# Kernel tuning notes

Measured on AMD Instinct MI355X. Metric: run time of the kernel, lower is better.

## Reference

```python
import jax, jax.numpy as jnp
import numpy as np

E = 1024      # embedding_size
H = 16        # num_heads
D = E // H    # head dim


def setup_inputs() -> dict:
    key = jax.random.key(0)
    k1, k2, k3, k4, k5 = jax.random.split(key, 5)
    x = jax.random.normal(k1, (4, 2048, E), dtype=jnp.float32)
    # nn.Linear(E, 3E): weight [3E, E], bias [3E]
    w_qkv = jax.random.normal(k2, (3 * E, E), dtype=jnp.float32) * (1.0 / np.sqrt(E))
    b_qkv = jax.random.normal(k3, (3 * E,), dtype=jnp.float32) * 0.02
    # nn.Linear(E, E)
    w_proj = jax.random.normal(k4, (E, E), dtype=jnp.float32) * (1.0 / np.sqrt(E))
    b_proj = jax.random.normal(k5, (E,), dtype=jnp.float32) * 0.02
    return {"x": x, "w_qkv": w_qkv, "b_qkv": b_qkv, "w_proj": w_proj, "b_proj": b_proj}


def reference(x, w_qkv, b_qkv, w_proj, b_proj):
    b, n, _ = x.shape
    qkv = x @ w_qkv.T + b_qkv                       # [b, n, 3E]
    # rearrange 'b n (h d qkv) -> qkv b h n d' : last dim grouped as (h, d, 3)
    qkv = qkv.reshape(b, n, H, D, 3)
    qkv = jnp.transpose(qkv, (4, 0, 2, 1, 3))        # [3, b, h, n, d]
    q, k, v = qkv[0], qkv[1], qkv[2]
    scale = 1.0 / np.sqrt(E / H)
    energy = jnp.einsum('bhqd,bhkd->bhqk', q, k) * scale
    attn = jax.nn.softmax(energy, axis=-1)
    out = jnp.einsum('bhqk,bhkd->bhqd', attn, v)     # [b, h, n, d]
    out = jnp.transpose(out, (0, 2, 1, 3)).reshape(b, n, E)
    return out @ w_proj.T + b_proj
```

## Files before the change

### kernel.cpp

```cpp
#include <hip/hip_runtime.h>
#include <hip/hip_fp16.h>

namespace {

constexpr int B = 4;
constexpr int N = 2048;
constexpr int E = 1024;
constexpr int H = 16;
constexpr int D = 64;
constexpr int M = B * N;

typedef __attribute__((ext_vector_type(8))) short bf16x8;
typedef __attribute__((ext_vector_type(8))) _Float16 f16x8;
typedef __attribute__((ext_vector_type(4))) _Float16 f16x4;
typedef __attribute__((ext_vector_type(4))) float f32x4;

__device__ inline ushort bf16_rne(float f) {
  unsigned u = __float_as_uint(f);
  return (ushort)((u + 0x7FFFu + ((u >> 16) & 1u)) >> 16);
}
__device__ inline void split2(float f, ushort& hi, ushort& lo) {
  unsigned u = __float_as_uint(f);
  hi = (ushort)(u >> 16);
  lo = bf16_rne(f - __uint_as_float(u & 0xFFFF0000u));
}

__global__ __launch_bounds__(256) void split_kernel(
    const float* __restrict__ in, ushort* __restrict__ hi,
    ushort* __restrict__ lo, int n4) {
  int i = blockIdx.x * blockDim.x + threadIdx.x;
  const int stride = gridDim.x * blockDim.x;
  for (; i < n4; i += stride) {
    const float4 f = ((const float4*)in)[i];
    ushort4 h, l;
    split2(f.x, h.x, l.x);
    split2(f.y, h.y, l.y);
    split2(f.z, h.z, l.z);
    split2(f.w, h.w, l.w);
    ((ushort4*)hi)[i] = h;
    ((ushort4*)lo)[i] = l;
  }
}

template <int MODE>
__global__ __launch_bounds__(256) void gemm_x3(
    const ushort* __restrict__ Ahg, const ushort* __restrict__ Alg,
    const ushort* __restrict__ Bhg, const ushort* __restrict__ Blg,
    const float* __restrict__ bias, ushort* __restrict__ qh,
    ushort* __restrict__ ql, ushort* __restrict__ kh, ushort* __restrict__ kl,
    ushort* __restrict__ vt, float* __restrict__ outp) {
  __shared__ ushort LAh[4096], LAl[4096], LBh[4096], LBl[4096];
  const int tid = threadIdx.x;
  const int l = tid & 63, wid = tid >> 6;
  const int wr = wid >> 1, wc = wid & 1;
  const int lr = l & 15, kg = l >> 4;
  const int m0 = blockIdx.x * 128, n0 = blockIdx.y * 128;

  f32x4 acc[4][4];
#pragma unroll
  for (int i = 0; i < 4; ++i)
#pragma unroll
    for (int j = 0; j < 4; ++j) acc[i][j] = (f32x4){0.f, 0.f, 0.f, 0.f};

  for (int k0 = 0; k0 < E; k0 += 32) {
    const ushort* gAh = Ahg + (size_t)m0 * E + k0;
    const ushort* gAl = Alg + (size_t)m0 * E + k0;
    const ushort* gBh = Bhg + (size_t)n0 * E + k0;
    const ushort* gBl = Blg + (size_t)n0 * E + k0;
    __syncthreads();
    auto stage = [&](const ushort* gp, ushort* lp, int half) {
      const int c = half * 256 + tid;
      __builtin_amdgcn_global_load_lds(
          (__attribute__((address_space(1))) void*)(gp + (size_t)(c >> 2) * E +
                                                    (c & 3) * 8),
          (__attribute__((address_space(3))) void*)(lp +
                                                    (half * 256 + (tid & ~63)) * 8),
          16, 0, 0);
    };
    stage(gAh, LAh, 0); stage(gAh, LAh, 1);
    stage(gAl, LAl, 0); stage(gAl, LAl, 1);
    stage(gBh, LBh, 0); stage(gBh, LBh, 1);
    stage(gBl, LBl, 0); stage(gBl, LBl, 1);
    __syncthreads();

    bf16x8 aH[4], aL[4], bH[4], bL[4];
#pragma unroll
    for (int rb = 0; rb < 4; ++rb) {
      const int off = (wr * 64 + rb * 16 + lr) * 32 + kg * 8;
      aH[rb] = *(const bf16x8*)(LAh + off);
      aL[rb] = *(const bf16x8*)(LAl + off);
    }
#pragma unroll
    for (int cb = 0; cb < 4; ++cb) {
      const int off = (wc * 64 + cb * 16 + lr) * 32 + kg * 8;
      bH[cb] = *(const bf16x8*)(LBh + off);
      bL[cb] = *(const bf16x8*)(LBl + off);
    }
#pragma unroll
    for (int rb = 0; rb < 4; ++rb)
#pragma unroll
      for (int cb = 0; cb < 4; ++cb) {
        acc[rb][cb] = __builtin_amdgcn_mfma_f32_16x16x32_bf16(
            aH[rb], bH[cb], acc[rb][cb], 0, 0, 0);
        acc[rb][cb] = __builtin_amdgcn_mfma_f32_16x16x32_bf16(
            aH[rb], bL[cb], acc[rb][cb], 0, 0, 0);
        acc[rb][cb] = __builtin_amdgcn_mfma_f32_16x16x32_bf16(
            aL[rb], bH[cb], acc[rb][cb], 0, 0, 0);
      }
  }

#pragma unroll
  for (int cb = 0; cb < 4; ++cb) {
    const int col = n0 + wc * 64 + cb * 16 + lr;
    const float bv = bias[col];
    if (MODE == 0) {
      const int h = col / 192;
      const int rem = col - h * 192;
      const int dd = rem / 3;
      const int s = rem - dd * 3;
      if (s == 2) {
#pragma unroll
        for (int rb = 0; rb < 4; ++rb) {
          const int m = m0 + wr * 64 + rb * 16 + kg * 4;
          const int bb = m >> 11, nn = m & (N - 1);
          f16x4 pk;
#pragma unroll
          for (int r = 0; r < 4; ++r)
            pk[r] = (_Float16)(acc[rb][cb][r] + bv);
          const size_t vidx =
              ((((size_t)bb * H + h) * (N / 64) + (nn >> 6)) * 64 + dd) * 64 +
              (nn & 63);
          *(f16x4*)((_Float16*)vt + vidx) = pk;
        }
      } else {
#pragma unroll
        for (int rb = 0; rb < 4; ++rb)
#pragma unroll
          for (int r = 0; r < 4; ++r) {
            const int m = m0 + wr * 64 + rb * 16 + kg * 4 + r;
            const int bb = m >> 11, nn = m & (N - 1);
            float v = acc[rb][cb][r] + bv;
            ushort hi, lo;
            const size_t idx = (((size_t)bb * H + h) * N + nn) * D + dd;
            if (s == 0) {
              v *= 0.125f;
              split2(v, hi, lo);
              qh[idx] = hi; ql[idx] = lo;
            } else {
              split2(v, hi, lo);
              kh[idx] = hi; kl[idx] = lo;
            }
          }
      }
    } else {
#pragma unroll
      for (int rb = 0; rb < 4; ++rb)
#pragma unroll
        for (int r = 0; r < 4; ++r) {
          const int m = m0 + wr * 64 + rb * 16 + kg * 4 + r;
          outp[(size_t)m * E + col] = acc[rb][cb][r] + bv;
        }
    }
  }
}

__global__ __launch_bounds__(256, 2) void attn_mfma(
    const ushort* __restrict__ Qh, const ushort* __restrict__ Ql,
    const ushort* __restrict__ Kh, const ushort* __restrict__ Kl,
    const ushort* __restrict__ Vt, ushort* __restrict__ Aoh,
    ushort* __restrict__ Aol) {
  __shared__ ushort KhL[2][4096], KlL[2][4096], VtL[2][4096], PsL[4][4096];
  const int tid = threadIdx.x;
  const int l = tid & 63, w = tid >> 6;
  const int lr = l & 15, g = l >> 4;
  const int bh = blockIdx.x, bb = bh >> 4, hh = bh & 15;
  const int q0 = blockIdx.y * 256 + w * 64;

  const int sr = tid >> 2;
  const int sc = tid & 3;
  const int slotA = sr * 8 + (sc ^ (sr & 7));
  const int slotB = sr * 8 + ((sc + 4) ^ (sr & 7));

  bf16x8 qfh[4][2], qfl[4][2];
#pragma unroll
  for (int rb = 0; rb < 4; ++rb)
#pragma unroll
    for (int ks = 0; ks < 2; ++ks) {
      const size_t off =
          ((size_t)bh * N + q0 + rb * 16 + lr) * D + ks * 32 + g * 8;
      qfh[rb][ks] = *(const bf16x8*)(Qh + off);
      qfl[rb][ks] = *(const bf16x8*)(Ql + off);
    }

  f32x4 o[4][4];
  float m_[4][4], l_[4][4];
#pragma unroll
  for (int rb = 0; rb < 4; ++rb)
#pragma unroll
    for (int r = 0; r < 4; ++r) {
      m_[rb][r] = -1e30f;
      l_[rb][r] = 0.f;
      o[rb][r] = (f32x4){0.f, 0.f, 0.f, 0.f};
    }

  ushort* Pw = &PsL[w][0];
  constexpr int NT = N / 64;

#define LOAD_SET(SET, KT)                                                     \
  do {                                                                        \
    const size_t ko = ((size_t)bh * N + (size_t)(KT) * 64 + sr) * 64;         \
    const size_t vo = (((size_t)bh * (N / 64) + (KT)) * 64 + sr) * 64;        \
    SET[0] = *(const uint4*)(Kh + ko + sc * 8);                               \
    SET[1] = *(const uint4*)(Kh + ko + (sc + 4) * 8);                         \
    SET[2] = *(const uint4*)(Kl + ko + sc * 8);                               \
    SET[3] = *(const uint4*)(Kl + ko + (sc + 4) * 8);                         \
    SET[4] = *(const uint4*)(Vt + vo + sc * 8);                               \
    SET[5] = *(const uint4*)(Vt + vo + (sc + 4) * 8);                         \
  } while (0)

#define WRITE_SET(SET, BUF)                                                   \
  do {                                                                        \
    *(uint4*)(&KhL[BUF][slotA * 8]) = SET[0];                                 \
    *(uint4*)(&KhL[BUF][slotB * 8]) = SET[1];                                 \
    *(uint4*)(&KlL[BUF][slotA * 8]) = SET[2];                                 \
    *(uint4*)(&KlL[BUF][slotB * 8]) = SET[3];                                 \
    *(uint4*)(&VtL[BUF][slotA * 8]) = SET[4];                                 \
    *(uint4*)(&VtL[BUF][slotB * 8]) = SET[5];                                 \
  } while (0)

  auto compute = [&](int buf) {
    const ushort* KhC = &KhL[buf][0];
    const ushort* KlC = &KlL[buf][0];
    const ushort* VtC = &VtL[buf][0];

    f32x4 s4[4][4];
#pragma unroll
    for (int rb = 0; rb < 4; ++rb)
#pragma unroll
      for (int cb = 0; cb < 4; ++cb) s4[rb][cb] = (f32x4){0.f, 0.f, 0.f, 0.f};
    __builtin_amdgcn_s_setprio(1);
#pragma unroll
    for (int ks = 0; ks < 2; ++ks) {
      bf16x8 kfh[4], kfl[4];
#pragma unroll
      for (int cb = 0; cb < 4; ++cb) {
        const int sl = (cb * 16 + lr) * 8 + ((ks * 4 + g) ^ (lr & 7));
        kfh[cb] = *(const bf16x8*)(KhC + sl * 8);
        kfl[cb] = *(const bf16x8*)(KlC + sl * 8);
      }
#pragma unroll
      for (int rb = 0; rb < 4; ++rb)
#pragma unroll
        for (int cb = 0; cb < 4; ++cb) {
          s4[rb][cb] = __builtin_amdgcn_mfma_f32_16x16x32_bf16(
              qfh[rb][ks], kfh[cb], s4[rb][cb], 0, 0, 0);
          s4[rb][cb] = __builtin_amdgcn_mfma_f32_16x16x32_bf16(
              qfh[rb][ks], kfl[cb], s4[rb][cb], 0, 0, 0);
          s4[rb][cb] = __builtin_amdgcn_mfma_f32_16x16x32_bf16(
              qfl[rb][ks], kfh[cb], s4[rb][cb], 0, 0, 0);
        }
    }
    __builtin_amdgcn_s_setprio(0);

#pragma unroll
    for (int rb = 0; rb < 4; ++rb)
#pragma unroll
      for (int r = 0; r < 4; ++r) {
        float mx = fmaxf(fmaxf(s4[rb][0][r], s4[rb][1][r]),
                         fmaxf(s4[rb][2][r], s4[rb][3][r]));
        mx = fmaxf(mx, __shfl_xor(mx, 1, 16));
        mx = fmaxf(mx, __shfl_xor(mx, 2, 16));
        mx = fmaxf(mx, __shfl_xor(mx, 4, 16));
        mx = fmaxf(mx, __shfl_xor(mx, 8, 16));
        const float mn = fmaxf(m_[rb][r], mx);
        const float fac = __expf(m_[rb][r] - mn);
        m_[rb][r] = mn;
        float sum = 0.f;
#pragma unroll
        for (int cb = 0; cb < 4; ++cb) {
          const float p = __expf(s4[rb][cb][r] - mn);
          s4[rb][cb][r] = p;
          sum += p;
        }
        sum += __shfl_xor(sum, 1, 16);
        sum += __shfl_xor(sum, 2, 16);
        sum += __shfl_xor(sum, 4, 16);
        sum += __shfl_xor(sum, 8, 16);
        l_[rb][r] = l_[rb][r] * fac + sum;
#pragma unroll
        for (int cb = 0; cb < 4; ++cb) o[rb][cb][r] *= fac;
        const int row = rb * 16 + g * 4 + r;
#pragma unroll
        for (int cb = 0; cb < 4; ++cb) {
          const int idx = (row * 64 + cb * 16 + lr) ^ ((row & 7) << 3);
          ((_Float16*)Pw)[idx] = (_Float16)s4[rb][cb][r];
        }
      }

    __builtin_amdgcn_s_setprio(1);
#pragma unroll
    for (int ks = 0; ks < 2; ++ks) {
      f16x8 pf[4], vf[4];
#pragma unroll
      for (int rb = 0; rb < 4; ++rb) {
        const int sl = (rb * 16 + lr) * 8 + ((ks * 4 + g) ^ (lr & 7));
        pf[rb] = *(const f16x8*)(Pw + sl * 8);
      }
#pragma unroll
      for (int cb = 0; cb < 4; ++cb) {
        const int sl = (cb * 16 + lr) * 8 + ((ks * 4 + g) ^ (lr & 7));
        vf[cb] = *(const f16x8*)(VtC + sl * 8);
      }
#pragma unroll
      for (int rb = 0; rb < 4; ++rb)
#pragma unroll
        for (int cb = 0; cb < 4; ++cb)
          o[rb][cb] = __builtin_amdgcn_mfma_f32_16x16x32_f16(
              pf[rb], vf[cb], o[rb][cb], 0, 0, 0);
    }
    __builtin_amdgcn_s_setprio(0);
  };

  uint4 sA[6], sB[6];
  LOAD_SET(sA, 0);

  for (int kt2 = 0; kt2 < NT; kt2 += 2) {
    asm volatile("s_waitcnt vmcnt(0)" ::: "memory");
    __builtin_amdgcn_s_barrier();
    WRITE_SET(sA, 0);
    if (kt2 + 1 < NT) LOAD_SET(sB, kt2 + 1);
    asm volatile("s_waitcnt lgkmcnt(0)" ::: "memory");
    __builtin_amdgcn_s_barrier();
    compute(0);
    asm volatile("s_waitcnt vmcnt(0)" ::: "memory");
    __builtin_amdgcn_s_barrier();
    WRITE_SET(sB, 1);
    if (kt2 + 2 < NT) LOAD_SET(sA, kt2 + 2);
    asm volatile("s_waitcnt lgkmcnt(0)" ::: "memory");
    __builtin_amdgcn_s_barrier();
    compute(1);
  }
#undef LOAD_SET
#undef WRITE_SET

#pragma unroll
  for (int rb = 0; rb < 4; ++rb)
#pragma unroll
    for (int r = 0; r < 4; ++r) {
      const float inv = 1.f / l_[rb][r];
      const int n = q0 + rb * 16 + g * 4 + r;
      const size_t base = ((size_t)bb * N + n) * E + hh * D;
#pragma unroll
      for (int cb = 0; cb < 4; ++cb) {
        ushort hi, lo;
        split2(o[rb][cb][r] * inv, hi, lo);
        Aoh[base + cb * 16 + lr] = hi;
        Aol[base + cb * 16 + lr] = lo;
      }
    }
}

}

extern "C" void kernel_launch(void* const* d_in, const int* in_sizes, int n_in,
                              void* d_out, int out_size, void* d_ws,
                              size_t ws_size, hipStream_t stream) {
  (void)in_sizes; (void)n_in; (void)out_size; (void)ws_size;
  const float* x      = (const float*)d_in[0];
  const float* w_qkv  = (const float*)d_in[1];
  const float* b_qkv  = (const float*)d_in[2];
  const float* w_proj = (const float*)d_in[3];
  const float* b_proj = (const float*)d_in[4];
  float* out = (float*)d_out;

  constexpr size_t MB = 1ull << 20;
  char* w = (char*)d_ws;
  ushort* xh  = (ushort*)(w + 0 * MB);
  ushort* xl  = (ushort*)(w + 16 * MB);
  ushort* wqh = (ushort*)(w + 32 * MB);
  ushort* wql = (ushort*)(w + 38 * MB);
  ushort* wph = (ushort*)(w + 44 * MB);
  ushort* wpl = (ushort*)(w + 46 * MB);
  ushort* Aoh = (ushort*)(w + 48 * MB);
  ushort* Aol = (ushort*)(w + 64 * MB);
  ushort* Qh  = (ushort*)(w + 80 * MB);
  ushort* Ql  = (ushort*)(w + 96 * MB);
  ushort* Kh  = (ushort*)(w + 112 * MB);
  ushort* Kl  = (ushort*)(w + 128 * MB);
  ushort* Vt  = (ushort*)(w + 144 * MB);

  split_kernel<<<2048, 256, 0, stream>>>(x, xh, xl, (M * E) / 4);
  split_kernel<<<1024, 256, 0, stream>>>(w_qkv, wqh, wql, (3 * E * E) / 4);
  split_kernel<<<512, 256, 0, stream>>>(w_proj, wph, wpl, (E * E) / 4);

  gemm_x3<0><<<dim3(M / 128, 3 * E / 128), 256, 0, stream>>>(
      xh, xl, wqh, wql, b_qkv, Qh, Ql, Kh, Kl, Vt, nullptr);

  attn_mfma<<<dim3(B * H, N / 256), 256, 0, stream>>>(Qh, Ql, Kh, Kl, Vt, Aoh,
                                                      Aol);

  gemm_x3<1><<<dim3(M / 128, E / 128), 256, 0, stream>>>(
      Aoh, Aol, wph, wpl, b_proj, nullptr, nullptr, nullptr, nullptr, nullptr,
      out);
}
```

Before: 1.057 ms.

## Restructure attention loop: single staging set, one barrier, half-tile online softmax

The two-tile unrolled loop with two staging register sets is replaced by a single-tile loop that keeps one set of prefetch registers. The loop now needs one barrier per tile instead of two, and double buffering is kept through kt&1. Each 64-key tile is processed as two 32-key halves, each with its own online-softmax update, so the score accumulators are halved. The aim is to cut register pressure and synchronisation. The cost is twice as many rescale and max/sum shuffle steps per tile.

```diff
diff --git a/kernel.cpp b/kernel.cpp
--- a/kernel.cpp
+++ b/kernel.cpp
@@ -206,139 +206,132 @@
   ushort* Pw = &PsL[w][0];
   constexpr int NT = N / 64;
 
-#define LOAD_SET(SET, KT)                                                     \
+#define LOAD_SET(KT)                                                          \
   do {                                                                        \
     const size_t ko = ((size_t)bh * N + (size_t)(KT) * 64 + sr) * 64;         \
     const size_t vo = (((size_t)bh * (N / 64) + (KT)) * 64 + sr) * 64;        \
-    SET[0] = *(const uint4*)(Kh + ko + sc * 8);                               \
-    SET[1] = *(const uint4*)(Kh + ko + (sc + 4) * 8);                         \
-    SET[2] = *(const uint4*)(Kl + ko + sc * 8);                               \
-    SET[3] = *(const uint4*)(Kl + ko + (sc + 4) * 8);                         \
-    SET[4] = *(const uint4*)(Vt + vo + sc * 8);                               \
-    SET[5] = *(const uint4*)(Vt + vo + (sc + 4) * 8);                         \
+    S[0] = *(const uint4*)(Kh + ko + sc * 8);                                 \
+    S[1] = *(const uint4*)(Kh + ko + (sc + 4) * 8);                           \
+    S[2] = *(const uint4*)(Kl + ko + sc * 8);                                 \
+    S[3] = *(const uint4*)(Kl + ko + (sc + 4) * 8);                           \
+    S[4] = *(const uint4*)(Vt + vo + sc * 8);                                 \
+    S[5] = *(const uint4*)(Vt + vo + (sc + 4) * 8);                           \
   } while (0)
 
-#define WRITE_SET(SET, BUF)                                                   \
+#define WRITE_SET(BUF)                                                        \
   do {                                                                        \
-    *(uint4*)(&KhL[BUF][slotA * 8]) = SET[0];                                 \
-    *(uint4*)(&KhL[BUF][slotB * 8]) = SET[1];                                 \
-    *(uint4*)(&KlL[BUF][slotA * 8]) = SET[2];                                 \
-    *(uint4*)(&KlL[BUF][slotB * 8]) = SET[3];                                 \
-    *(uint4*)(&VtL[BUF][slotA * 8]) = SET[4];                                 \
-    *(uint4*)(&VtL[BUF][slotB * 8]) = SET[5];                                 \
+    *(uint4*)(&KhL[BUF][slotA * 8]) = S[0];                                   \
+    *(uint4*)(&KhL[BUF][slotB * 8]) = S[1];                                   \
+    *(uint4*)(&KlL[BUF][slotA * 8]) = S[2];                                   \
+    *(uint4*)(&KlL[BUF][slotB * 8]) = S[3];                                   \
+    *(uint4*)(&VtL[BUF][slotA * 8]) = S[4];                                   \
+    *(uint4*)(&VtL[BUF][slotB * 8]) = S[5];                                   \
   } while (0)
 
-  auto compute = [&](int buf) {
+  uint4 S[6];
+  LOAD_SET(0);
+
+  for (int kt = 0; kt < NT; ++kt) {
+    const int buf = kt & 1;
+    asm volatile("s_waitcnt vmcnt(0)" ::: "memory");
+    WRITE_SET(buf);
+    if (kt + 1 < NT) LOAD_SET(kt + 1);
+    asm volatile("s_waitcnt lgkmcnt(0)" ::: "memory");
+    __builtin_amdgcn_s_barrier();
+
     const ushort* KhC = &KhL[buf][0];
     const ushort* KlC = &KlL[buf][0];
     const ushort* VtC = &VtL[buf][0];
 
-    f32x4 s4[4][4];
-#pragma unroll
-    for (int rb = 0; rb < 4; ++rb)
-#pragma unroll
-      for (int cb = 0; cb < 4; ++cb) s4[rb][cb] = (f32x4){0.f, 0.f, 0.f, 0.f};
-    __builtin_amdgcn_s_setprio(1);
-#pragma unroll
-    for (int ks = 0; ks < 2; ++ks) {
-      bf16x8 kfh[4], kfl[4];
-#pragma unroll
-      for (int cb = 0; cb < 4; ++cb) {
-        const int sl = (cb * 16 + lr) * 8 + ((ks * 4 + g) ^ (lr & 7));
-        kfh[cb] = *(const bf16x8*)(KhC + sl * 8);
-        kfl[cb] = *(const bf16x8*)(KlC + sl * 8);
-      }
+#pragma unroll
+    for (int half = 0; half < 2; ++half) {
+      f32x4 s4[4][2];
 #pragma unroll
       for (int rb = 0; rb < 4; ++rb)
 #pragma unroll
+        for (int c2 = 0; c2 < 2; ++c2) s4[rb][c2] = (f32x4){0.f, 0.f, 0.f, 0.f};
+      __builtin_amdgcn_s_setprio(1);
+#pragma unroll
+      for (int ks = 0; ks < 2; ++ks) {
+        bf16x8 kfh[2], kfl[2];
+#pragma unroll
+        for (int c2 = 0; c2 < 2; ++c2) {
+          const int cb = half * 2 + c2;
+          const int sl = (cb * 16 + lr) * 8 + ((ks * 4 + g) ^ (lr & 7));
+          kfh[c2] = *(const bf16x8*)(KhC + sl * 8);
+          kfl[c2] = *(const bf16x8*)(KlC + sl * 8);
+        }
+#pragma unroll
+        for (int rb = 0; rb < 4; ++rb)
+#pragma unroll
+          for (int c2 = 0; c2 < 2; ++c2) {
+            s4[rb][c2] = __builtin_amdgcn_mfma_f32_16x16x32_bf16(
+                qfh[rb][ks], kfh[c2], s4[rb][c2], 0, 0, 0);
+            s4[rb][c2] = __builtin_amdgcn_mfma_f32_16x16x32_bf16(
+                qfh[rb][ks], kfl[c2], s4[rb][c2], 0, 0, 0);
+            s4[rb][c2] = __builtin_amdgcn_mfma_f32_16x16x32_bf16(
+                qfl[rb][ks], kfh[c2], s4[rb][c2], 0, 0, 0);
+          }
+      }
+      __builtin_amdgcn_s_setprio(0);
+
+#pragma unroll
+      for (int rb = 0; rb < 4; ++rb)
+#pragma unroll
+        for (int r = 0; r < 4; ++r) {
+          float mx = fmaxf(s4[rb][0][r], s4[rb][1][r]);
+          mx = fmaxf(mx, __shfl_xor(mx, 1, 16));
+          mx = fmaxf(mx, __shfl_xor(mx, 2, 16));
+          mx = fmaxf(mx, __shfl_xor(mx, 4, 16));
+          mx = fmaxf(mx, __shfl_xor(mx, 8, 16));
+          const float mn = fmaxf(m_[rb][r], mx);
+          const float fac = __expf(m_[rb][r] - mn);
+          m_[rb][r] = mn;
+          float sum = 0.f;
+#pragma unroll
+          for (int c2 = 0; c2 < 2; ++c2) {
+            const float p = __expf(s4[rb][c2][r] - mn);
+            s4[rb][c2][r] = p;
+            sum += p;
+          }
+          sum += __shfl_xor(sum, 1, 16);
+          sum += __shfl_xor(sum, 2, 16);
+          sum += __shfl_xor(sum, 4, 16);
+          sum += __shfl_xor(sum, 8, 16);
+          l_[rb][r] = l_[rb][r] * fac + sum;
+#pragma unroll
+          for (int cb = 0; cb < 4; ++cb) o[rb][cb][r] *= fac;
+          const int row = rb * 16 + g * 4 + r;
+#pragma unroll
+          for (int c2 = 0; c2 < 2; ++c2) {
+            const int cb = half * 2 + c2;
+            const int idx = (row * 64 + cb * 16 + lr) ^ ((row & 7) << 3);
+            ((_Float16*)Pw)[idx] = (_Float16)s4[rb][c2][r];
+          }
+        }
+
+      __builtin_amdgcn_s_setprio(1);
+      {
+        f16x8 pf[4], vf[4];
+#pragma unroll
+        for (int rb = 0; rb < 4; ++rb) {
+          const int sl = (rb * 16 + lr) * 8 + ((half * 4 + g) ^ (lr & 7));
+          pf[rb] = *(const f16x8*)(Pw + sl * 8);
+        }
+#pragma unroll
         for (int cb = 0; cb < 4; ++cb) {
-          s4[rb][cb] = __builtin_amdgcn_mfma_f32_16x16x32_bf16(
-              qfh[rb][ks], kfh[cb], s4[rb][cb], 0, 0, 0);
-          s4[rb][cb] = __builtin_amdgcn_mfma_f32_16x16x32_bf16(
-              qfh[rb][ks], kfl[cb], s4[rb][cb], 0, 0, 0);
-          s4[rb][cb] = __builtin_amdgcn_mfma_f32_16x16x32_bf16(
-              qfl[rb][ks], kfh[cb], s4[rb][cb], 0, 0, 0);
-        }
-    }
-    __builtin_amdgcn_s_setprio(0);
-
-#pragma unroll
-    for (int rb = 0; rb < 4; ++rb)
-#pragma unroll
-      for (int r = 0; r < 4; ++r) {
-        float mx = fmaxf(fmaxf(s4[rb][0][r], s4[rb][1][r]),
-                         fmaxf(s4[rb][2][r], s4[rb][3][r]));
-        mx = fmaxf(mx, __shfl_xor(mx, 1, 16));
-        mx = fmaxf(mx, __shfl_xor(mx, 2, 16));
-        mx = fmaxf(mx, __shfl_xor(mx, 4, 16));
-        mx = fmaxf(mx, __shfl_xor(mx, 8, 16));
-        const float mn = fmaxf(m_[rb][r], mx);
-        const float fac = __expf(m_[rb][r] - mn);
-        m_[rb][r] = mn;
-        float sum = 0.f;
-#pragma unroll
-        for (int cb = 0; cb < 4; ++cb) {
-          const float p = __expf(s4[rb][cb][r] - mn);
-          s4[rb][cb][r] = p;
-          sum += p;
-        }
-        sum += __shfl_xor(sum, 1, 16);
-        sum += __shfl_xor(sum, 2, 16);
-        sum += __shfl_xor(sum, 4, 16);
-        sum += __shfl_xor(sum, 8, 16);
-        l_[rb][r] = l_[rb][r] * fac + sum;
-#pragma unroll
-        for (int cb = 0; cb < 4; ++cb) o[rb][cb][r] *= fac;
-        const int row = rb * 16 + g * 4 + r;
-#pragma unroll
-        for (int cb = 0; cb < 4; ++cb) {
-          const int idx = (row * 64 + cb * 16 + lr) ^ ((row & 7) << 3);
-          ((_Float16*)Pw)[idx] = (_Float16)s4[rb][cb][r];
-        }
-      }
-
-    __builtin_amdgcn_s_setprio(1);
-#pragma unroll
-    for (int ks = 0; ks < 2; ++ks) {
-      f16x8 pf[4], vf[4];
-#pragma unroll
-      for (int rb = 0; rb < 4; ++rb) {
-        const int sl = (rb * 16 + lr) * 8 + ((ks * 4 + g) ^ (lr & 7));
-        pf[rb] = *(const f16x8*)(Pw + sl * 8);
-      }
-#pragma unroll
-      for (int cb = 0; cb < 4; ++cb) {
-        const int sl = (cb * 16 + lr) * 8 + ((ks * 4 + g) ^ (lr & 7));
-        vf[cb] = *(const f16x8*)(VtC + sl * 8);
-      }
-#pragma unroll
-      for (int rb = 0; rb < 4; ++rb)
-#pragma unroll
-        for (int cb = 0; cb < 4; ++cb)
-          o[rb][cb] = __builtin_amdgcn_mfma_f32_16x16x32_f16(
-              pf[rb], vf[cb], o[rb][cb], 0, 0, 0);
-    }
-    __builtin_amdgcn_s_setprio(0);
-  };
-
-  uint4 sA[6], sB[6];
-  LOAD_SET(sA, 0);
-
-  for (int kt2 = 0; kt2 < NT; kt2 += 2) {
-    asm volatile("s_waitcnt vmcnt(0)" ::: "memory");
-    __builtin_amdgcn_s_barrier();
-    WRITE_SET(sA, 0);
-    if (kt2 + 1 < NT) LOAD_SET(sB, kt2 + 1);
-    asm volatile("s_waitcnt lgkmcnt(0)" ::: "memory");
-    __builtin_amdgcn_s_barrier();
-    compute(0);
-    asm volatile("s_waitcnt vmcnt(0)" ::: "memory");
-    __builtin_amdgcn_s_barrier();
-    WRITE_SET(sB, 1);
-    if (kt2 + 2 < NT) LOAD_SET(sA, kt2 + 2);
-    asm volatile("s_waitcnt lgkmcnt(0)" ::: "memory");
-    __builtin_amdgcn_s_barrier();
-    compute(1);
+          const int sl = (cb * 16 + lr) * 8 + ((half * 4 + g) ^ (lr & 7));
+          vf[cb] = *(const f16x8*)(VtC + sl * 8);
+        }
+#pragma unroll
+        for (int rb = 0; rb < 4; ++rb)
+#pragma unroll
+          for (int cb = 0; cb < 4; ++cb)
+            o[rb][cb] = __builtin_amdgcn_mfma_f32_16x16x32_f16(
+                pf[rb], vf[cb], o[rb][cb], 0, 0, 0);
+      }
+      __builtin_amdgcn_s_setprio(0);
+    }
   }
 #undef LOAD_SET
 #undef WRITE_SET
```

Measured after the change: 1.282 ms. 1.21x slower.
